# Kernel optimization log

Hardware: AMD Instinct MI355X
Metric: run time of the kernel (lower is better)

## Reference

```python
import jax, jax.numpy as jnp
import numpy as np

RADIUS = 2
MAXDISP = 192


def _lga(x, g, radius=RADIUS):
    """Local guided aggregation (GANet LGA).
    x: [B, D, H, W] cost volume. g: [B, 3*k*k, H, W] L1-normalized guidance.
    out[b,d,p] = sum_off g0[off,p]*x[d,p+off] + g1[off,p]*x[d-1,p+off] + g2[off,p]*x[d+1,p+off]
    """
    B, D, H, W = x.shape
    k = 2 * radius + 1
    g0, g1, g2 = jnp.split(g, 3, axis=1)  # each [B, k*k, H, W]
    pad_sp = ((0, 0), (0, 0), (radius, radius), (radius, radius))
    x_p = jnp.pad(x, pad_sp)
    # disparity-shifted volumes (zero padded at the ends)
    x_dm = jnp.pad(x, ((0, 0), (1, 0), (0, 0), (0, 0)))[:, :D]   # x[d-1]
    x_dp = jnp.pad(x, ((0, 0), (0, 1), (0, 0), (0, 0)))[:, 1:]   # x[d+1]
    xm_p = jnp.pad(x_dm, pad_sp)
    xp_p = jnp.pad(x_dp, pad_sp)
    out = jnp.zeros_like(x)
    idx = 0
    for i in range(k):
        for j in range(k):
            sl = (slice(None), slice(None), slice(i, i + H), slice(j, j + W))
            out = out + (x_p[sl] * g0[:, idx][:, None]
                         + xm_p[sl] * g1[:, idx][:, None]
                         + xp_p[sl] * g2[:, idx][:, None])
            idx += 1
    return out


def _forward(x, lg1, conv_w):
    B = x.shape[0]
    H8, W8 = x.shape[3] * 8, x.shape[4] * 8
    # conv32x1: 3x3x3 conv, 32 -> 1 channels, padding 1, no bias
    x = jax.lax.conv_general_dilated(
        x, conv_w, window_strides=(1, 1, 1), padding=[(1, 1)] * 3,
        dimension_numbers=("NCDHW", "OIDHW", "NCDHW"))  # [B,1,D,H/8,W/8]
    # trilinear upsample (align_corners=False / half-pixel centers)
    x = jax.image.resize(x, (B, 1, MAXDISP + 1, H8, W8), method="linear")
    x = jnp.squeeze(x, 1)  # [B, D+1, H, W]
    # L1-normalize guidance over channel dim (F.normalize p=1 dim=1)
    g = lg1 / jnp.maximum(jnp.sum(jnp.abs(lg1), axis=1, keepdims=True), 1e-12)
    # LGA2 = local guided aggregation applied twice with the same guidance
    x = _lga(x, g)
    x = _lga(x, g)
    # softmin over disparity, then L1 normalize over disparity
    p = jax.nn.softmax(-x, axis=1)
    p = p / jnp.maximum(jnp.sum(jnp.abs(p), axis=1, keepdims=True), 1e-12)
    disps = jnp.arange(MAXDISP + 1, dtype=p.dtype)
    return jnp.einsum("bdhw,d->bhw", p, disps)


def setup_inputs() -> dict:
    key = jax.random.key(0)
    k1, k2, k3 = jax.random.split(key, 3)
    x = jax.random.normal(k1, (1, 32, 49, 32, 64), dtype=jnp.float32)
    lg1 = jax.random.uniform(k2, (1, 75, 256, 512), dtype=jnp.float32)
    conv_w = jax.random.normal(k3, (1, 32, 3, 3, 3), dtype=jnp.float32) * 0.05
    return {"x": x, "lg1": lg1, "conv_w": conv_w}


def reference(x, lg1, conv_w):
    return _forward(x, lg1, conv_w)
```

## Files before the change

kernel.cpp:

```cpp
#include <hip/hip_runtime.h>
#include <hip/hip_bf16.h>

#define DIN 49
#define HIN 32
#define WIN 64
#define CIN 32
#define DOUT 193
#define HOUT 256
#define WOUT 512
#define NPIX (HOUT * WOUT)
#define NUPS (DOUT * NPIX)
#define NCONV (DIN * HIN * WIN)
#define NZ 1
#define CGRP 8

#define ROWSTRIDE 33
#define PIXW 10
#define SUWORDS (20 * ROWSTRIDE * PIXW)
#define CHUNK 16
#define NPL 18
#define JGUARD(k, tid) ((k) < 5 || (tid) < 160)

typedef __attribute__((ext_vector_type(2))) float v2f;

__device__ __forceinline__ float dot2bf(unsigned a, unsigned b, float c) {
    float d;
    asm("v_dot2_f32_bf16 %0, %1, %2, %3"
        : "=v"(d)
        : "v"(a), "v"(b), "v"(c));
    return d;
}

__global__ void conv3d_kernel(const float* __restrict__ x,
                              const float* __restrict__ w,
                              float* __restrict__ partial) {
    __shared__ float ws[4 * 27];
    const int grp = blockIdx.y;
    for (int t = threadIdx.x; t < 4 * 27; t += blockDim.x)
        ws[t] = w[grp * (4 * 27) + t];
    __syncthreads();

    int idx4 = blockIdx.x * blockDim.x + threadIdx.x;
    int w4 = idx4 & 15;
    int t2 = idx4 >> 4;
    int hq = t2 & 31;
    int dq = t2 >> 5;
    int wq0 = w4 * 4;

    float acc0 = 0.f, acc1 = 0.f, acc2 = 0.f, acc3 = 0.f;
    const float* xg = x + (size_t)grp * 4 * NCONV;
#pragma unroll
    for (int cl = 0; cl < 4; ++cl) {
        const float* xb = xg + cl * NCONV;
        const float* wb = ws + cl * 27;
#pragma unroll
        for (int kd = 0; kd < 3; ++kd) {
            int zd = dq + kd - 1;
            if (zd < 0 || zd >= DIN) continue;
#pragma unroll
            for (int kh = 0; kh < 3; ++kh) {
                int zh = hq + kh - 1;
                if (zh < 0 || zh >= HIN) continue;
                const float* row = xb + (zd * HIN + zh) * WIN;
                float4 v = *(const float4*)(row + wq0);
                float xl = (wq0 > 0) ? row[wq0 - 1] : 0.f;
                float xr = (wq0 < WIN - 4) ? row[wq0 + 4] : 0.f;
                float w0 = wb[(kd * 3 + kh) * 3 + 0];
                float w1 = wb[(kd * 3 + kh) * 3 + 1];
                float w2 = wb[(kd * 3 + kh) * 3 + 2];
                acc0 = fmaf(w0, xl, acc0);
                acc0 = fmaf(w1, v.x, acc0);
                acc0 = fmaf(w2, v.y, acc0);
                acc1 = fmaf(w0, v.x, acc1);
                acc1 = fmaf(w1, v.y, acc1);
                acc1 = fmaf(w2, v.z, acc1);
                acc2 = fmaf(w0, v.y, acc2);
                acc2 = fmaf(w1, v.z, acc2);
                acc2 = fmaf(w2, v.w, acc2);
                acc3 = fmaf(w0, v.z, acc3);
                acc3 = fmaf(w1, v.w, acc3);
                acc3 = fmaf(w2, xr, acc3);
            }
        }
    }
    float4 o4 = make_float4(acc0, acc1, acc2, acc3);
    *(float4*)(partial + (size_t)grp * NCONV + (size_t)idx4 * 4) = o4;
}

__global__ void convfold_kernel(const float* __restrict__ partial,
                                float* __restrict__ c) {
    int i4 = blockIdx.x * blockDim.x + threadIdx.x;
    float4 s = *(const float4*)(partial + (size_t)i4 * 4);
#pragma unroll
    for (int g = 1; g < CGRP; ++g) {
        float4 v = *(const float4*)(partial + (size_t)g * NCONV +
                                    (size_t)i4 * 4);
        s.x += v.x;
        s.y += v.y;
        s.z += v.z;
        s.w += v.w;
    }
    *(float4*)(c + (size_t)i4 * 4) = s;
}

__device__ __forceinline__ unsigned short bf16bits(float f) {
    __hip_bfloat16 h = __float2bfloat16(f);
    unsigned short b;
    __builtin_memcpy(&b, &h, 2);
    return b;
}

#define TAP16(sp, t)                                                 \
    do {                                                             \
        unsigned u0, u1, u2, u3, u4, u5, u6, u7, u8;                 \
        { uint2 q = *(const uint2*)(sp);       u0 = q.x; u1 = q.y; } \
        { uint2 q = *(const uint2*)((sp) + 2); u2 = q.x; u3 = q.y; } \
        { uint2 q = *(const uint2*)((sp) + 4); u4 = q.x; u5 = q.y; } \
        { uint2 q = *(const uint2*)((sp) + 6); u6 = q.x; u7 = q.y; } \
        u8 = (sp)[8];                                                \
        const unsigned g0w = gp[(t) >> 1];                           \
        const unsigned g1w = gp[(25 + (t)) >> 1];                    \
        const unsigned g2w = gp[(50 + (t)) >> 1];                    \
        unsigned W10, W2z, Wz1, W02;                                 \
        if ((t) & 1) {                                               \
            W10 = (g1w & 0xFFFFu) | (g0w & 0xFFFF0000u);             \
            W2z = g2w >> 16;                                         \
            Wz1 = g1w << 16;                                         \
            W02 = (g0w >> 16) | (g2w & 0xFFFF0000u);                 \
        } else {                                                     \
            W10 = (g1w >> 16) | (g0w << 16);                         \
            W2z = g2w & 0xFFFFu;                                     \
            Wz1 = g1w & 0xFFFF0000u;                                 \
            W02 = (g0w & 0xFFFFu) | (g2w << 16);                     \
        }                                                            \
        acc[0] = dot2bf(u0, W10, acc[0]);                            \
        acc[0] = dot2bf(u1, W2z, acc[0]);                            \
        acc[1] = dot2bf(u0, Wz1, acc[1]);                            \
        acc[1] = dot2bf(u1, W02, acc[1]);                            \
        acc[2] = dot2bf(u1, W10, acc[2]);                            \
        acc[2] = dot2bf(u2, W2z, acc[2]);                            \
        acc[3] = dot2bf(u1, Wz1, acc[3]);                            \
        acc[3] = dot2bf(u2, W02, acc[3]);                            \
        acc[4] = dot2bf(u2, W10, acc[4]);                            \
        acc[4] = dot2bf(u3, W2z, acc[4]);                            \
        acc[5] = dot2bf(u2, Wz1, acc[5]);                            \
        acc[5] = dot2bf(u3, W02, acc[5]);                            \
        acc[6] = dot2bf(u3, W10, acc[6]);                            \
        acc[6] = dot2bf(u4, W2z, acc[6]);                            \
        acc[7] = dot2bf(u3, Wz1, acc[7]);                            \
        acc[7] = dot2bf(u4, W02, acc[7]);                            \
        acc[8] = dot2bf(u4, W10, acc[8]);                            \
        acc[8] = dot2bf(u5, W2z, acc[8]);                            \
        acc[9] = dot2bf(u4, Wz1, acc[9]);                            \
        acc[9] = dot2bf(u5, W02, acc[9]);                            \
        acc[10] = dot2bf(u5, W10, acc[10]);                          \
        acc[10] = dot2bf(u6, W2z, acc[10]);                          \
        acc[11] = dot2bf(u5, Wz1, acc[11]);                          \
        acc[11] = dot2bf(u6, W02, acc[11]);                          \
        acc[12] = dot2bf(u6, W10, acc[12]);                          \
        acc[12] = dot2bf(u7, W2z, acc[12]);                          \
        acc[13] = dot2bf(u6, Wz1, acc[13]);                          \
        acc[13] = dot2bf(u7, W02, acc[13]);                          \
        acc[14] = dot2bf(u7, W10, acc[14]);                          \
        acc[14] = dot2bf(u8, W2z, acc[14]);                          \
        acc[15] = dot2bf(u7, Wz1, acc[15]);                          \
        acc[15] = dot2bf(u8, W02, acc[15]);                          \
    } while (0)

#define TAPTAIL(sp, t)                                               \
    do {                                                             \
        unsigned u0 = (sp)[0];                                       \
        const unsigned g0w = gp[(t) >> 1];                           \
        const unsigned g1w = gp[(25 + (t)) >> 1];                    \
        unsigned W10;                                                \
        if ((t) & 1)                                                 \
            W10 = (g1w & 0xFFFFu) | (g0w & 0xFFFF0000u);             \
        else                                                         \
            W10 = (g1w >> 16) | (g0w << 16);                         \
        acc0 = dot2bf(u0, W10, acc0);                                \
    } while (0)

__device__ __forceinline__ void jdec(int j, int& seg, int& dl, int& r) {
    seg = j & 3;
    int rowjob = j >> 2;
    dl = rowjob / 20;
    r = rowjob - dl * 20;
}

__device__ __forceinline__ void stageA1(const float* __restrict__ cvol,
                                        int tid, int h0p, int w0p, int dstart,
                                        unsigned (&aq0)[6], unsigned (&aq2)[3]) {
    aq2[0] = 0u;
    aq2[1] = 0u;
    aq2[2] = 0u;
#pragma unroll
    for (int k = 0; k < 6; ++k) {
        const bool a = JGUARD(k, tid);
        int j = tid + k * 256;
        int seg, dl, r;
        jdec(j, seg, dl, r);
        int gh = h0p - 2 + r;
        int gwb = w0p - 8 + seg * 8;
        int gd = dstart - 1 + dl;
        if (a && gd >= 0 && gd < DOUT && gh >= 0 && gh < HOUT && gwb >= 0 &&
            (gwb + 8) <= WOUT) {
            float fd = (gd + 0.5f) * (49.0f / 193.0f) - 0.5f;
            fd = fminf(fmaxf(fd, 0.f), (float)(DIN - 1));
            int d0c = min((int)fd, DIN - 2);
            float ad = fd - (float)d0c;
            float fh = (gh + 0.5f) * 0.125f - 0.5f;
            fh = fminf(fmaxf(fh, 0.f), (float)(HIN - 1));
            int h0c = min((int)fh, HIN - 2);
            float ah = fh - (float)h0c;
            int g = gwb >> 3;
            int cm1 = max(g - 1, 0);
            int cp1 = min(g + 1, WIN - 1);
            const float* p00 = cvol + (d0c * HIN + h0c) * WIN;
            const float* p01 = p00 + WIN;
            const float* p10 = p00 + HIN * WIN;
            const float* p11 = p10 + WIN;
            float q00, q01, q10, q11, a0, a1, a2;
            q00 = p00[cm1]; q01 = p01[cm1];
            q10 = p10[cm1]; q11 = p11[cm1];
            a0 = (q00 + ah * (q01 - q00)) * (1.f - ad) +
                 (q10 + ah * (q11 - q10)) * ad;
            q00 = p00[g]; q01 = p01[g];
            q10 = p10[g]; q11 = p11[g];
            a1 = (q00 + ah * (q01 - q00)) * (1.f - ad) +
                 (q10 + ah * (q11 - q10)) * ad;
            q00 = p00[cp1]; q01 = p01[cp1];
            q10 = p10[cp1]; q11 = p11[cp1];
            a2 = (q00 + ah * (q01 - q00)) * (1.f - ad) +
                 (q10 + ah * (q11 - q10)) * ad;
            aq0[k] = (unsigned)bf16bits(a0) | ((unsigned)bf16bits(a1) << 16);
            aq2[k >> 1] |= ((unsigned)bf16bits(a2)) << ((k & 1) * 16);
        } else {
            aq0[k] = 0u;
        }
    }
}

__device__ __forceinline__ void scat1(unsigned short* __restrict__ su16,
                                      int tid, const unsigned (&aq0)[6],
                                      const unsigned (&aq2)[3]) {
#pragma unroll
    for (int k = 0; k < 6; ++k) {
        if (JGUARD(k, tid)) {
            int j = tid + k * 256;
            int seg, dl, r;
            jdec(j, seg, dl, r);
            int hb = (r * ROWSTRIDE + seg * 8) * (2 * PIXW) + dl;
            float a0 = __uint_as_float(aq0[k] << 16);
            float a1 = __uint_as_float(aq0[k] & 0xFFFF0000u);
            float a2 = __uint_as_float((k & 1) ? (aq2[k >> 1] & 0xFFFF0000u)
                                               : (aq2[k >> 1] << 16));
            float d01 = a1 - a0, d12 = a2 - a1;
            su16[hb + 0 * 2 * PIXW] = bf16bits(a0 + 0.5625f * d01);
            su16[hb + 1 * 2 * PIXW] = bf16bits(a0 + 0.6875f * d01);
            su16[hb + 2 * 2 * PIXW] = bf16bits(a0 + 0.8125f * d01);
            su16[hb + 3 * 2 * PIXW] = bf16bits(a0 + 0.9375f * d01);
            su16[hb + 4 * 2 * PIXW] = bf16bits(a1 + 0.0625f * d12);
            su16[hb + 5 * 2 * PIXW] = bf16bits(a1 + 0.1875f * d12);
            su16[hb + 6 * 2 * PIXW] = bf16bits(a1 + 0.3125f * d12);
            su16[hb + 7 * 2 * PIXW] = bf16bits(a1 + 0.4375f * d12);
        }
    }
}

__device__ __forceinline__ void stageA2(const unsigned short* __restrict__ xus,
                                        int tid, int h0p, int w0p, int dstart,
                                        uint4 (&dat)[6]) {
#pragma unroll
    for (int k = 0; k < 6; ++k) {
        const bool a = JGUARD(k, tid);
        int j = tid + k * 256;
        int seg, dl, r;
        jdec(j, seg, dl, r);
        int gh = h0p - 2 + r;
        int gwb = w0p - 8 + seg * 8;
        int gd = dstart - 1 + dl;
        uint4 v = make_uint4(0u, 0u, 0u, 0u);
        if (a && gd >= 0 && gd < DOUT && gh >= 0 && gh < HOUT && gwb >= 0 &&
            (gwb + 8) <= WOUT)
            v = *(const uint4*)(xus + (size_t)gd * NPIX + gh * WOUT + gwb);
        dat[k] = v;
    }
}

__device__ __forceinline__ void scat2(unsigned short* __restrict__ su16,
                                      int tid, const uint4 (&dat)[6]) {
#pragma unroll
    for (int k = 0; k < 6; ++k) {
        if (JGUARD(k, tid)) {
            int j = tid + k * 256;
            int seg, dl, r;
            jdec(j, seg, dl, r);
            int hb = (r * ROWSTRIDE + seg * 8) * (2 * PIXW) + dl;
            su16[hb + 0 * 2 * PIXW] = (unsigned short)(dat[k].x);
            su16[hb + 1 * 2 * PIXW] = (unsigned short)(dat[k].x >> 16);
            su16[hb + 2 * 2 * PIXW] = (unsigned short)(dat[k].y);
            su16[hb + 3 * 2 * PIXW] = (unsigned short)(dat[k].y >> 16);
            su16[hb + 4 * 2 * PIXW] = (unsigned short)(dat[k].z);
            su16[hb + 5 * 2 * PIXW] = (unsigned short)(dat[k].z >> 16);
            su16[hb + 6 * 2 * PIXW] = (unsigned short)(dat[k].w);
            su16[hb + 7 * 2 * PIXW] = (unsigned short)(dat[k].w >> 16);
        }
    }
}

__global__ __launch_bounds__(256)
__attribute__((amdgpu_num_vgpr(128))) void lga1_kernel(
    const float* __restrict__ cvol,
    const float* __restrict__ lg1,
    __hip_bfloat16* __restrict__ yout) {
    const int tid = threadIdx.x;
    const int tx = tid & 15;
    const int ty = tid >> 4;
    const int w0p = blockIdx.x * 16;
    const int h0p = blockIdx.y * 16;
    const int pix = (h0p + ty) * WOUT + (w0p + tx);

    __shared__ __align__(16) unsigned su[2 * SUWORDS];

    unsigned aq0[6], aq2[3];
    stageA1(cvol, tid, h0p, w0p, 0, aq0, aq2);

    float asum = 0.f;
    unsigned gp[38];
#pragma unroll
    for (int p = 0; p < 38; ++p) {
        int c0 = 2 * p, c1 = 2 * p + 1;
        float w0 = lg1[c0 * NPIX + pix];
        float w1 = (c1 < 75) ? lg1[c1 * NPIX + pix] : 0.f;
        unsigned b0 = bf16bits(w0), b1 = bf16bits(w1);
        asum += fabsf(__uint_as_float(b0 << 16)) +
                fabsf(__uint_as_float(b1 << 16));
        gp[p] = b0 | (b1 << 16);
    }
    const float inv = 1.f / fmaxf(asum, 1e-12f);

    const int pbase = (ty * ROWSTRIDE + tx + 6) * PIXW;
    __hip_bfloat16* ybase = yout + pix;

    scat1((unsigned short*)su, tid, aq0, aq2);
    int pb = 0;
    for (int d0 = 0; d0 + CHUNK < DOUT; d0 += CHUNK) {
        __syncthreads();
        stageA1(cvol, tid, h0p, w0p, d0 + CHUNK, aq0, aq2);

        const unsigned* sw = su + pb * SUWORDS + pbase;
        float acc[16];
#pragma unroll
        for (int d = 0; d < 16; ++d) acc[d] = 0.f;
        __builtin_amdgcn_s_setprio(1);
#pragma unroll
        for (int i = 0; i < 5; ++i) {
#pragma unroll
            for (int j = 0; j < 5; ++j) {
                const int t = i * 5 + j;
                TAP16(sw + (i * ROWSTRIDE + j) * PIXW, t);
            }
        }
        __builtin_amdgcn_s_setprio(0);

        scat1((unsigned short*)(su + (pb ^ 1) * SUWORDS), tid, aq0, aq2);

#pragma unroll
        for (int dd = 0; dd < CHUNK; ++dd)
            ybase[(size_t)(d0 + dd) * NPIX] = __float2bfloat16(acc[dd] * inv);
        pb ^= 1;
    }

    __syncthreads();
    {
        const unsigned* sw = su + pb * SUWORDS + pbase;
        float acc0 = 0.f;
#pragma unroll
        for (int i = 0; i < 5; ++i) {
#pragma unroll
            for (int j = 0; j < 5; ++j) {
                const int t = i * 5 + j;
                TAPTAIL(sw + (i * ROWSTRIDE + j) * PIXW, t);
            }
        }
        ybase[(size_t)192 * NPIX] = __float2bfloat16(acc0 * inv);
    }
}

__global__ __launch_bounds__(256)
__attribute__((amdgpu_num_vgpr(128))) void lga2_kernel(
    const __hip_bfloat16* __restrict__ xin,
    const float* __restrict__ lg1,
    float* __restrict__ out) {
    const int tid = threadIdx.x;
    const int tx = tid & 15;
    const int ty = tid >> 4;
    const int w0p = blockIdx.x * 16;
    const int h0p = blockIdx.y * 16;
    const int pix = (h0p + ty) * WOUT + (w0p + tx);
    const unsigned short* xus = (const unsigned short*)xin;

    __shared__ __align__(16) unsigned su[2 * SUWORDS];

    uint4 dat[6];
    stageA2(xus, tid, h0p, w0p, 0, dat);

    float asum = 0.f;
    unsigned gp[38];
#pragma unroll
    for (int p = 0; p < 38; ++p) {
        int c0 = 2 * p, c1 = 2 * p + 1;
        float w0 = lg1[c0 * NPIX + pix];
        float w1 = (c1 < 75) ? lg1[c1 * NPIX + pix] : 0.f;
        unsigned b0 = bf16bits(w0), b1 = bf16bits(w1);
        asum += fabsf(__uint_as_float(b0 << 16)) +
                fabsf(__uint_as_float(b1 << 16));
        gp[p] = b0 | (b1 << 16);
    }
    const float inv = 1.f / fmaxf(asum, 1e-12f);

    const int pbase = (ty * ROWSTRIDE + tx + 6) * PIXW;

    float m = -1e30f, l = 0.f, s_acc = 0.f;

    scat2((unsigned short*)su, tid, dat);
    int pb = 0;
    for (int d0 = 0; d0 + CHUNK < DOUT; d0 += CHUNK) {
        __syncthreads();
        stageA2(xus, tid, h0p, w0p, d0 + CHUNK, dat);

        const unsigned* sw = su + pb * SUWORDS + pbase;
        float acc[16];
#pragma unroll
        for (int d = 0; d < 16; ++d) acc[d] = 0.f;
        __builtin_amdgcn_s_setprio(1);
#pragma unroll
        for (int i = 0; i < 5; ++i) {
#pragma unroll
            for (int j = 0; j < 5; ++j) {
                const int t = i * 5 + j;
                TAP16(sw + (i * ROWSTRIDE + j) * PIXW, t);
            }
        }
        __builtin_amdgcn_s_setprio(0);

        scat2((unsigned short*)(su + (pb ^ 1) * SUWORDS), tid, dat);

        {
            float v[16];
            float mx = m;
#pragma unroll
            for (int d = 0; d < 16; ++d) {
                v[d] = -acc[d] * inv;
                mx = fmaxf(mx, v[d]);
            }
            float sc = __expf(m - mx);
            float sum = 0.f, ssum = 0.f;
#pragma unroll
            for (int d = 0; d < 16; ++d) {
                float e = __expf(v[d] - mx);
                sum += e;
                ssum += e * (float)(d0 + d);
            }
            l = l * sc + sum;
            s_acc = s_acc * sc + ssum;
            m = mx;
        }
        pb ^= 1;
    }

    __syncthreads();
    {
        const unsigned* sw = su + pb * SUWORDS + pbase;
        float acc0 = 0.f;
#pragma unroll
        for (int i = 0; i < 5; ++i) {
#pragma unroll
            for (int j = 0; j < 5; ++j) {
                const int t = i * 5 + j;
                TAPTAIL(sw + (i * ROWSTRIDE + j) * PIXW, t);
            }
        }
        float vv = -acc0 * inv;
        float mx = fmaxf(m, vv);
        float sc = __expf(m - mx);
        float e = __expf(vv - mx);
        l = l * sc + e;
        s_acc = s_acc * sc + e * 192.f;
    }

    out[pix] = s_acc / l;
}

extern "C" void kernel_launch(void* const* d_in, const int* in_sizes, int n_in,
                              void* d_out, int out_size, void* d_ws,
                              size_t ws_size, hipStream_t stream) {
    const float* x = (const float*)d_in[0];
    const float* lg1 = (const float*)d_in[1];
    const float* cw = (const float*)d_in[2];
    float* out = (float*)d_out;

    float* c = (float*)d_ws;
    __hip_bfloat16* regA = (__hip_bfloat16*)((char*)d_ws + (size_t)NCONV * 4);
    __hip_bfloat16* y1 = regA + (size_t)NUPS;
    float* cpart = (float*)y1;

    dim3 cgrid(NCONV / 1024, CGRP);
    conv3d_kernel<<<cgrid, 256, 0, stream>>>(x, cw, cpart);
    convfold_kernel<<<NCONV / 1024, 256, 0, stream>>>(cpart, c);

    dim3 grid(WOUT / 16, HOUT / 16, NZ);
    lga1_kernel<<<grid, 256, 0, stream>>>(c, lg1, y1);
    lga2_kernel<<<grid, 256, 0, stream>>>(y1, lg1, out);
}
```

Before: 282.3 us.

## Split disparity range across two z-blocks with partial softmax reduction

Both LGA kernels now split the 193 disparities into two halves handled by separate blocks, doubling the grid to raise occupancy and parallelism. The second kernel writes unnormalized exp-sums and weighted sums per half, and a new small kernel combines them. The running-max stabilisation of the softmin is removed, which relies on the cost values staying small enough not to overflow exp. Each block now reloads and normalizes the full guidance weights, adding redundant memory traffic and an extra launch.

```diff
diff --git a/kernel.cpp b/kernel.cpp
--- a/kernel.cpp
+++ b/kernel.cpp
@@ -11,7 +11,8 @@
 #define NPIX (HOUT * WOUT)
 #define NUPS (DOUT * NPIX)
 #define NCONV (DIN * HIN * WIN)
-#define NZ 1
+#define NZ 2
+#define ZSPAN 96
 #define CGRP 8
 
 #define ROWSTRIDE 33
@@ -318,12 +319,14 @@
     const int ty = tid >> 4;
     const int w0p = blockIdx.x * 16;
     const int h0p = blockIdx.y * 16;
+    const int zb = blockIdx.z * ZSPAN;
+    const bool lastz = (blockIdx.z == NZ - 1);
     const int pix = (h0p + ty) * WOUT + (w0p + tx);
 
     __shared__ __align__(16) unsigned su[2 * SUWORDS];
 
     unsigned aq0[6], aq2[3];
-    stageA1(cvol, tid, h0p, w0p, 0, aq0, aq2);
+    stageA1(cvol, tid, h0p, w0p, zb, aq0, aq2);
 
     float asum = 0.f;
     unsigned gp[38];
@@ -344,9 +347,11 @@
 
     scat1((unsigned short*)su, tid, aq0, aq2);
     int pb = 0;
-    for (int d0 = 0; d0 + CHUNK < DOUT; d0 += CHUNK) {
+    for (int d0 = zb; d0 < zb + ZSPAN; d0 += CHUNK) {
         __syncthreads();
-        stageA1(cvol, tid, h0p, w0p, d0 + CHUNK, aq0, aq2);
+        const bool hn = lastz ? (d0 + CHUNK < DOUT)
+                              : (d0 + CHUNK < zb + ZSPAN);
+        if (hn) stageA1(cvol, tid, h0p, w0p, d0 + CHUNK, aq0, aq2);
 
         const unsigned* sw = su + pb * SUWORDS + pbase;
         float acc[16];
@@ -363,7 +368,8 @@
         }
         __builtin_amdgcn_s_setprio(0);
 
-        scat1((unsigned short*)(su + (pb ^ 1) * SUWORDS), tid, aq0, aq2);
+        if (hn) scat1((unsigned short*)(su + (pb ^ 1) * SUWORDS), tid, aq0,
+                      aq2);
 
 #pragma unroll
         for (int dd = 0; dd < CHUNK; ++dd)
@@ -371,8 +377,8 @@
         pb ^= 1;
     }
 
-    __syncthreads();
-    {
+    if (lastz) {
+        __syncthreads();
         const unsigned* sw = su + pb * SUWORDS + pbase;
         float acc0 = 0.f;
 #pragma unroll
@@ -391,19 +397,21 @@
 __attribute__((amdgpu_num_vgpr(128))) void lga2_kernel(
     const __hip_bfloat16* __restrict__ xin,
     const float* __restrict__ lg1,
-    float* __restrict__ out) {
+    float* __restrict__ part) {
     const int tid = threadIdx.x;
     const int tx = tid & 15;
     const int ty = tid >> 4;
     const int w0p = blockIdx.x * 16;
     const int h0p = blockIdx.y * 16;
+    const int zb = blockIdx.z * ZSPAN;
+    const bool lastz = (blockIdx.z == NZ - 1);
     const int pix = (h0p + ty) * WOUT + (w0p + tx);
     const unsigned short* xus = (const unsigned short*)xin;
 
     __shared__ __align__(16) unsigned su[2 * SUWORDS];
 
     uint4 dat[6];
-    stageA2(xus, tid, h0p, w0p, 0, dat);
+    stageA2(xus, tid, h0p, w0p, zb, dat);
 
     float asum = 0.f;
     unsigned gp[38];
@@ -421,13 +429,15 @@
 
     const int pbase = (ty * ROWSTRIDE + tx + 6) * PIXW;
 
-    float m = -1e30f, l = 0.f, s_acc = 0.f;
+    float l = 0.f, s_acc = 0.f;
 
     scat2((unsigned short*)su, tid, dat);
     int pb = 0;
-    for (int d0 = 0; d0 + CHUNK < DOUT; d0 += CHUNK) {
+    for (int d0 = zb; d0 < zb + ZSPAN; d0 += CHUNK) {
         __syncthreads();
-        stageA2(xus, tid, h0p, w0p, d0 + CHUNK, dat);
+        const bool hn = lastz ? (d0 + CHUNK < DOUT)
+                              : (d0 + CHUNK < zb + ZSPAN);
+        if (hn) stageA2(xus, tid, h0p, w0p, d0 + CHUNK, dat);
 
         const unsigned* sw = su + pb * SUWORDS + pbase;
         float acc[16];
@@ -444,33 +454,24 @@
         }
         __builtin_amdgcn_s_setprio(0);
 
-        scat2((unsigned short*)(su + (pb ^ 1) * SUWORDS), tid, dat);
+        if (hn) scat2((unsigned short*)(su + (pb ^ 1) * SUWORDS), tid, dat);
 
         {
-            float v[16];
-            float mx = m;
+            float sum = 0.f, ssum = 0.f;
 #pragma unroll
             for (int d = 0; d < 16; ++d) {
-                v[d] = -acc[d] * inv;
-                mx = fmaxf(mx, v[d]);
-            }
-            float sc = __expf(m - mx);
-            float sum = 0.f, ssum = 0.f;
-#pragma unroll
-            for (int d = 0; d < 16; ++d) {
-                float e = __expf(v[d] - mx);
+                float e = __expf(-acc[d] * inv);
                 sum += e;
                 ssum += e * (float)(d0 + d);
             }
-            l = l * sc + sum;
-            s_acc = s_acc * sc + ssum;
-            m = mx;
+            l += sum;
+            s_acc += ssum;
         }
         pb ^= 1;
     }
 
-    __syncthreads();
-    {
+    if (lastz) {
+        __syncthreads();
         const unsigned* sw = su + pb * SUWORDS + pbase;
         float acc0 = 0.f;
 #pragma unroll
@@ -481,15 +482,22 @@
                 TAPTAIL(sw + (i * ROWSTRIDE + j) * PIXW, t);
             }
         }
-        float vv = -acc0 * inv;
-        float mx = fmaxf(m, vv);
-        float sc = __expf(m - mx);
-        float e = __expf(vv - mx);
-        l = l * sc + e;
-        s_acc = s_acc * sc + e * 192.f;
-    }
-
-    out[pix] = s_acc / l;
+        float e = __expf(-acc0 * inv);
+        l += e;
+        s_acc += e * 192.f;
+    }
+
+    float* pz = part + (size_t)blockIdx.z * 2 * NPIX;
+    pz[pix] = l;
+    pz[NPIX + pix] = s_acc;
+}
+
+__global__ void reduce2_kernel(const float* __restrict__ part,
+                               float* __restrict__ out) {
+    int pix = blockIdx.x * blockDim.x + threadIdx.x;
+    float L = part[pix] + part[2 * NPIX + pix];
+    float S = part[NPIX + pix] + part[3 * NPIX + pix];
+    out[pix] = S / L;
 }
 
 extern "C" void kernel_launch(void* const* d_in, const int* in_sizes, int n_in,
@@ -504,6 +512,7 @@
     __hip_bfloat16* regA = (__hip_bfloat16*)((char*)d_ws + (size_t)NCONV * 4);
     __hip_bfloat16* y1 = regA + (size_t)NUPS;
     float* cpart = (float*)y1;
+    float* part = (float*)regA;
 
     dim3 cgrid(NCONV / 1024, CGRP);
     conv3d_kernel<<<cgrid, 256, 0, stream>>>(x, cw, cpart);
@@ -511,5 +520,7 @@
 
     dim3 grid(WOUT / 16, HOUT / 16, NZ);
     lga1_kernel<<<grid, 256, 0, stream>>>(c, lg1, y1);
-    lga2_kernel<<<grid, 256, 0, stream>>>(y1, lg1, out);
-}
+    lga2_kernel<<<grid, 256, 0, stream>>>(y1, lg1, part);
+
+    reduce2_kernel<<<NPIX / 256, 256, 0, stream>>>(part, out);
+}
```

Result: slower. 298.2 us (+5.6%).
